# Kernel tuning notes

Measured on AMD Instinct MI355X. Metric: run time of the kernel, lower is better.

The kernel has to match this reference:

```python
import jax, jax.numpy as jnp
import numpy as np

D_EMBED = 1024
N_HEADS = 16
BATCH = 2
SEQ = 2048


def setup_inputs() -> dict:
    key = jax.random.key(0)
    k1, k2, k3 = jax.random.split(key, 3)
    scale = 0.02
    x = jax.random.normal(k1, (BATCH, SEQ, D_EMBED), dtype=jnp.float32)
    w_qkv = jax.random.normal(k2, (D_EMBED, 3 * D_EMBED), dtype=jnp.float32) * scale
    b_qkv = jnp.zeros((3 * D_EMBED,), dtype=jnp.float32)
    w_o = jax.random.normal(k3, (D_EMBED, D_EMBED), dtype=jnp.float32) * scale
    b_o = jnp.zeros((D_EMBED,), dtype=jnp.float32)
    return {"x": x, "w_qkv": w_qkv, "b_qkv": b_qkv, "w_o": w_o, "b_o": b_o}


def reference(x, w_qkv, b_qkv, w_o, b_o):
    bs, sl, ed = x.shape
    nh = N_HEADS
    hd = ed // nh
    # fused QKV projection, split into q, k, v
    qkv = x @ w_qkv + b_qkv                      # [bs, sl, 3*ed]
    q, k, v = jnp.split(qkv, 3, axis=2)
    # [bs, sl, (nh hd)] -> [bs, nh, sl, hd]
    def heads(t):
        return t.reshape(bs, sl, nh, hd).transpose(0, 2, 1, 3)
    q, k, v = heads(q), heads(k), heads(v)
    # scaled dot-product attention with causal mask (full SxS scores, as in the original)
    scores = jnp.einsum('bhqd,bhkd->bhqk', q, k) / jnp.sqrt(jnp.float32(hd))
    causal = jnp.tril(jnp.ones((sl, sl), dtype=bool))
    scores = jnp.where(causal[None, None, :, :], scores, jnp.float32(-jnp.inf))
    attn = jax.nn.softmax(scores, axis=-1)       # dropout p=0 -> identity
    out = jnp.einsum('bhqk,bhkd->bhqd', attn, v) # [bs, nh, sl, hd]
    out = out.transpose(0, 2, 1, 3).reshape(bs, sl, ed)
    return out @ w_o + b_o
```

## Files before the change

kernel.cpp:

```cpp
#include <hip/hip_runtime.h>
#include <hip/hip_bf16.h>

typedef __hip_bfloat16 bf16;
typedef unsigned short u16;
typedef __attribute__((ext_vector_type(8))) short short8;
typedef __attribute__((ext_vector_type(4))) float floatx4;

#define D_EMBED 1024
#define N_HEADS 16
#define HEAD_DIM 64
#define BATCH 2
#define SEQ 2048
#define ROWS (BATCH * SEQ)
#define QKV_COLS (3 * D_EMBED)
#define QSCALE 0.1803368801f

__device__ __forceinline__ void g2l16(const void* g, void* l) {
    __builtin_amdgcn_global_load_lds(
        (const __attribute__((address_space(1))) unsigned int*)g,
        (__attribute__((address_space(3))) unsigned int*)l,
        16, 0, 0);
}

__device__ __forceinline__ u16 f2b_bits(float f) {
    bf16 h = __float2bfloat16(f);
    u16 u;
    __builtin_memcpy(&u, &h, 2);
    return u;
}

__device__ __forceinline__ unsigned pack2(float a, float b) {
    return (unsigned)f2b_bits(a) | ((unsigned)f2b_bits(b) << 16);
}

__device__ __forceinline__ float fexp2(float x) {
#if __has_builtin(__builtin_amdgcn_exp2f)
    return __builtin_amdgcn_exp2f(x);
#else
    return exp2f(x);
#endif
}

__device__ __forceinline__ unsigned permpack(float a, float b) {
#if __has_builtin(__builtin_amdgcn_perm)
    return __builtin_amdgcn_perm(__float_as_uint(b), __float_as_uint(a), 0x07060302u);
#else
    return (__float_as_uint(a) >> 16) | (__float_as_uint(b) & 0xFFFF0000u);
#endif
}

__global__ __launch_bounds__(256)
void prep(const float* __restrict__ x, const float* __restrict__ w_qkv,
          const float* __restrict__ w_o, bf16* __restrict__ xb,
          bf16* __restrict__ wqkvT, bf16* __restrict__ woT)
{
    __shared__ u16 T[64][72];
    const int tid = threadIdx.x;
    const int bid = blockIdx.x;

    if (bid < 4096) {
        const int i = bid * 256 + tid;
        const float4 v = reinterpret_cast<const float4*>(x)[i];
        ushort4 o;
        o.x = f2b_bits(v.x); o.y = f2b_bits(v.y);
        o.z = f2b_bits(v.z); o.w = f2b_bits(v.w);
        reinterpret_cast<ushort4*>(xb)[i] = o;
        return;
    }
    const float* in; u16* out; int R, C, bx, by;
    if (bid < 4864) {
        const int t = bid - 4096;
        in = w_qkv; out = reinterpret_cast<u16*>(wqkvT); R = 1024; C = 3072;
        bx = t % 48; by = t / 48;
    } else {
        const int t = bid - 4864;
        in = w_o; out = reinterpret_cast<u16*>(woT); R = 1024; C = 1024;
        bx = t % 16; by = t / 16;
    }
    const int r0 = by * 64, c0 = bx * 64;
#pragma unroll
    for (int it = 0; it < 4; ++it) {
        const int r = (tid >> 4) + it * 16;
        const int c4 = (tid & 15) * 4;
        const float4 v = *reinterpret_cast<const float4*>(in + (size_t)(r0 + r) * C + c0 + c4);
        T[c4 + 0][r] = f2b_bits(v.x);
        T[c4 + 1][r] = f2b_bits(v.y);
        T[c4 + 2][r] = f2b_bits(v.z);
        T[c4 + 3][r] = f2b_bits(v.w);
    }
    __syncthreads();
#pragma unroll
    for (int it = 0; it < 4; ++it) {
        const int rr = (tid >> 4) + it * 16;
        const int cc4 = (tid & 15) * 4;
        ushort4 o = *reinterpret_cast<const ushort4*>(&T[rr][cc4]);
        *reinterpret_cast<ushort4*>(out + (size_t)(c0 + rr) * R + r0 + cc4) = o;
    }
}

__global__ __launch_bounds__(256)
void gemm_qkv(const bf16* __restrict__ A, const bf16* __restrict__ Bt,
              const float* __restrict__ bias,
              bf16* __restrict__ qb, bf16* __restrict__ kb, bf16* __restrict__ vtb)
{
    __shared__ __align__(16) char smem[16384];
    char* As = smem;
    char* Bs = smem + 8192;

    const int tid = threadIdx.x;
    const int lane = tid & 63, w = tid >> 6;
    const int quad = lane >> 4, l15 = lane & 15;
    const int mw = (w >> 1) * 64, nw = (w & 1) * 64;
    const int blockM = blockIdx.y * 128, blockN = blockIdx.x * 128;

    floatx4 acc[4][4];
#pragma unroll
    for (int i = 0; i < 4; ++i)
#pragma unroll
        for (int j = 0; j < 4; ++j) acc[i][j] = (floatx4){0.f, 0.f, 0.f, 0.f};

    for (int k0 = 0; k0 < 1024; k0 += 32) {
        __syncthreads();
#pragma unroll
        for (int it = 0; it < 2; ++it) {
            const int p = it * 256 + tid;
            const int row = p >> 2, ch = p & 3;
            char* dst = As + (it * 256 + (tid & ~63)) * 16;
            g2l16(A + (size_t)(blockM + row) * 1024 + k0 + ch * 8, dst);
            g2l16(Bt + (size_t)(blockN + row) * 1024 + k0 + ch * 8, dst + 8192);
        }
        __syncthreads();

        short8 af[4], bfr[4];
#pragma unroll
        for (int mi = 0; mi < 4; ++mi)
            af[mi] = *reinterpret_cast<const short8*>(
                As + (mw + mi * 16 + l15) * 64 + quad * 16);
#pragma unroll
        for (int ni = 0; ni < 4; ++ni)
            bfr[ni] = *reinterpret_cast<const short8*>(
                Bs + (nw + ni * 16 + l15) * 64 + quad * 16);
#pragma unroll
        for (int mi = 0; mi < 4; ++mi)
#pragma unroll
            for (int ni = 0; ni < 4; ++ni)
                acc[mi][ni] = __builtin_amdgcn_mfma_f32_16x16x32_bf16(
                    af[mi], bfr[ni], acc[mi][ni], 0, 0, 0);
    }

    __syncthreads();
    u16* W = reinterpret_cast<u16*>(smem + w * 2304);
    const bool isq = (blockN < 1024);
    const bool isv = (blockN >= 2048);

    float bvn[4];
#pragma unroll
    for (int ni = 0; ni < 4; ++ni) bvn[ni] = bias[blockN + nw + ni * 16 + l15];

    if (!isv) {
        bf16* dstbuf = isq ? qb : kb;
        const int coloff = blockN - (isq ? 0 : 1024);
#pragma unroll
        for (int mi = 0; mi < 4; ++mi) {
#pragma unroll
            for (int ni = 0; ni < 4; ++ni) {
#pragma unroll
                for (int r = 0; r < 4; ++r) {
                    float val = acc[mi][ni][r] + bvn[ni];
                    if (isq) val *= QSCALE;
                    W[(quad * 4 + r) * 72 + ni * 16 + l15] = f2b_bits(val);
                }
            }
#pragma unroll
            for (int half = 0; half < 2; ++half) {
                const int idx = half * 64 + lane;
                const int rowL = idx >> 3, ch = idx & 7;
                short8 v = *reinterpret_cast<const short8*>(W + rowL * 72 + ch * 8);
                const int grow = blockM + mw + mi * 16 + rowL;
                const int gcol = coloff + nw + ch * 8;
                *reinterpret_cast<short8*>(
                    reinterpret_cast<u16*>(dstbuf) + (size_t)grow * 1024 + gcol) = v;
            }
        }
    } else {
        const int col0 = blockN - 2048 + nw;
        const int h = col0 >> 6;
        const int bh = (blockM >> 11) * 16 + h;
        const int sb = (blockM & 2047) + mw;
        u16* vdst = reinterpret_cast<u16*>(vtb) + (size_t)bh * 64 * SEQ;
#pragma unroll
        for (int mi = 0; mi < 4; ++mi) {
#pragma unroll
            for (int ni = 0; ni < 4; ++ni) {
#pragma unroll
                for (int r = 0; r < 4; ++r)
                    W[(quad * 4 + r) * 72 + ni * 16 + l15] =
                        f2b_bits(acc[mi][ni][r] + bvn[ni]);
            }
#pragma unroll
            for (int mc = 0; mc < 2; ++mc) {
                u16 tmp[8];
#pragma unroll
                for (int e = 0; e < 8; ++e) tmp[e] = W[(mc * 8 + e) * 72 + lane];
                const int s = sb + mi * 16 + mc * 8;
                *reinterpret_cast<short8*>(vdst + (size_t)lane * SEQ + s) =
                    *reinterpret_cast<const short8*>(tmp);
            }
        }
    }
}

__global__ __launch_bounds__(256)
void gemm_out(const bf16* __restrict__ A, const bf16* __restrict__ Bt,
              const float* __restrict__ bias, float* __restrict__ outf)
{
    __shared__ __align__(16) char smem[12288];
    char* As = smem;
    char* Bs = smem + 8192;

    const int tid = threadIdx.x;
    const int lane = tid & 63, w = tid >> 6;
    const int quad = lane >> 4, l15 = lane & 15;
    const int mw = (w >> 1) * 64, nw = (w & 1) * 32;
    const int blockM = blockIdx.y * 128, blockN = blockIdx.x * 64;

    floatx4 acc[4][2];
#pragma unroll
    for (int i = 0; i < 4; ++i)
#pragma unroll
        for (int j = 0; j < 2; ++j) acc[i][j] = (floatx4){0.f, 0.f, 0.f, 0.f};

    for (int k0 = 0; k0 < 1024; k0 += 32) {
        __syncthreads();
#pragma unroll
        for (int it = 0; it < 2; ++it) {
            const int p = it * 256 + tid;
            const int row = p >> 2, ch = p & 3;
            g2l16(A + (size_t)(blockM + row) * 1024 + k0 + ch * 8,
                  As + (it * 256 + (tid & ~63)) * 16);
        }
        {
            const int row = tid >> 2, ch = tid & 3;
            g2l16(Bt + (size_t)(blockN + row) * 1024 + k0 + ch * 8,
                  Bs + (tid & ~63) * 16);
        }
        __syncthreads();

        short8 af[4], bfr[2];
#pragma unroll
        for (int mi = 0; mi < 4; ++mi)
            af[mi] = *reinterpret_cast<const short8*>(
                As + (mw + mi * 16 + l15) * 64 + quad * 16);
#pragma unroll
        for (int ni = 0; ni < 2; ++ni)
            bfr[ni] = *reinterpret_cast<const short8*>(
                Bs + (nw + ni * 16 + l15) * 64 + quad * 16);
#pragma unroll
        for (int mi = 0; mi < 4; ++mi)
#pragma unroll
            for (int ni = 0; ni < 2; ++ni)
                acc[mi][ni] = __builtin_amdgcn_mfma_f32_16x16x32_bf16(
                    af[mi], bfr[ni], acc[mi][ni], 0, 0, 0);
    }

    float bvn[2];
#pragma unroll
    for (int ni = 0; ni < 2; ++ni) bvn[ni] = bias[blockN + nw + ni * 16 + l15];

#pragma unroll
    for (int mi = 0; mi < 4; ++mi)
#pragma unroll
        for (int r = 0; r < 4; ++r) {
            const int row = blockM + mw + mi * 16 + quad * 4 + r;
#pragma unroll
            for (int ni = 0; ni < 2; ++ni) {
                const int col = blockN + nw + ni * 16 + l15;
                outf[(size_t)row * 1024 + col] = acc[mi][ni][r] + bvn[ni];
            }
        }
}

__global__ __launch_bounds__(256)
void attn_mfma(const bf16* __restrict__ qb, const bf16* __restrict__ kb,
               const bf16* __restrict__ vtb, bf16* __restrict__ ob)
{
    __shared__ __align__(16) char smem[40960];
    char* KV0 = smem;
    char* KV1 = smem + 16384;
    const int tid = threadIdx.x;
    const int lane = tid & 63, w = tid >> 6;
    const int quad = lane >> 4, l15 = lane & 15;
    char* Ps = smem + 32768 + w * 2048;

    const int pi = blockIdx.x;
    const int bh = blockIdx.y;
    const int b = bh >> 4, h = bh & 15;

    const int qtS = pi, qtB = 31 - pi;
    const int q0S = qtS * 64, q0B = qtB * 64;
    const int KT = qtB + 1;
    const int qrowS = q0S + w * 16 + l15;
    const int qrowB = q0B + w * 16 + l15;

    const size_t kvrow = (size_t)b * SEQ;
    const size_t vbase = (size_t)bh * 64 * SEQ;

    const short8 ones = {0x3F80, 0x3F80, 0x3F80, 0x3F80,
                         0x3F80, 0x3F80, 0x3F80, 0x3F80};

    const int row0 = tid >> 3;
    const int lch = (tid & 7) ^ (row0 & 7);
    const int loff0 = (tid & ~63) * 16;
    const int loff1 = loff0 + 4096;
    const bf16* ksrc0 = kb + (kvrow + row0) * D_EMBED + h * 64 + lch * 8;
    const bf16* ksrc1 = ksrc0 + (size_t)32 * D_EMBED;
    const bf16* vsrc0 = vtb + vbase + (size_t)row0 * SEQ + lch * 8;
    const bf16* vsrc1 = vsrc0 + (size_t)32 * SEQ;

    {
        const bf16* qsrcS = qb + (kvrow + q0S + row0) * D_EMBED + h * 64 + lch * 8;
        const bf16* qsrcB = qb + (kvrow + q0B + row0) * D_EMBED + h * 64 + lch * 8;
        g2l16(qsrcS, KV1 + loff0);
        g2l16(qsrcS + (size_t)32 * D_EMBED, KV1 + loff1);
        g2l16(qsrcB, KV1 + 8192 + loff0);
        g2l16(qsrcB + (size_t)32 * D_EMBED, KV1 + 8192 + loff1);
        g2l16(ksrc0, KV0 + loff0);
        g2l16(ksrc1, KV0 + loff1);
        g2l16(vsrc0, KV0 + 8192 + loff0);
        g2l16(vsrc1, KV0 + 8192 + loff1);
    }
    __syncthreads();

    const int qoff = (w * 16 + l15) * 128;
    const int x0 = (quad ^ (l15 & 7)) * 16;
    const int x1 = ((quad + 4) ^ (l15 & 7)) * 16;
    const short8 qS0 = *reinterpret_cast<const short8*>(KV1 + qoff + x0);
    const short8 qS1 = *reinterpret_cast<const short8*>(KV1 + qoff + x1);
    const short8 qB0 = *reinterpret_cast<const short8*>(KV1 + 8192 + qoff + x0);
    const short8 qB1 = *reinterpret_cast<const short8*>(KV1 + 8192 + qoff + x1);
    __syncthreads();

    floatx4 OaccS[4], OaccB[4], LaccS, LaccB;
#pragma unroll
    for (int i = 0; i < 4; ++i) {
        OaccS[i] = (floatx4){0.f, 0.f, 0.f, 0.f};
        OaccB[i] = (floatx4){0.f, 0.f, 0.f, 0.f};
    }
    LaccS = (floatx4){0.f, 0.f, 0.f, 0.f};
    LaccB = (floatx4){0.f, 0.f, 0.f, 0.f};

    auto prefetch = [&](int nkt, char* dst) {
        const size_t ko = (size_t)nkt * 64;
        g2l16(ksrc0 + ko * D_EMBED, dst + loff0);
        g2l16(ksrc1 + ko * D_EMBED, dst + loff1);
        g2l16(vsrc0 + ko, dst + 8192 + loff0);
        g2l16(vsrc1 + ko, dst + 8192 + loff1);
    };

    auto compute = [&](int kt, char* Ks, char* Vs) {
        const int k0 = kt * 64;
        short8 kf[2][4], vf[2][4];
#pragma unroll
        for (int ms = 0; ms < 4; ++ms) {
            const int roff = (ms * 16 + l15) * 128;
            kf[0][ms] = *reinterpret_cast<const short8*>(Ks + roff + x0);
            kf[1][ms] = *reinterpret_cast<const short8*>(Ks + roff + x1);
        }
#pragma unroll
        for (int ks = 0; ks < 2; ++ks)
#pragma unroll
            for (int ds = 0; ds < 4; ++ds)
                vf[ks][ds] = *reinterpret_cast<const short8*>(
                    Vs + (ds * 16 + l15) * 128 + (((quad + ks * 4) ^ (l15 & 7)) * 16));

        {
            floatx4 S[4];
#pragma unroll
            for (int ms = 0; ms < 4; ++ms) {
                floatx4 t = (floatx4){0.f, 0.f, 0.f, 0.f};
                t = __builtin_amdgcn_mfma_f32_16x16x32_bf16(kf[0][ms], qB0, t, 0, 0, 0);
                S[ms] = __builtin_amdgcn_mfma_f32_16x16x32_bf16(kf[1][ms], qB1, t, 0, 0, 0);
            }
            const bool diag = (kt == KT - 1);
#pragma unroll
            for (int ms = 0; ms < 4; ++ms) {
                float p[4];
#pragma unroll
                for (int r = 0; r < 4; ++r) {
                    float s = S[ms][r];
                    if (diag && (k0 + ms * 16 + quad * 4 + r) > qrowB) s = -1e30f;
                    p[r] = fexp2(s);
                }
                const int k = ms * 16 + quad * 4;
                uint2 pw;
                pw.x = permpack(p[0], p[1]);
                pw.y = permpack(p[2], p[3]);
                *reinterpret_cast<uint2*>(Ps + (k >> 3) * 256 + l15 * 16 + (k & 7) * 2) = pw;
            }
#pragma unroll
            for (int ks = 0; ks < 2; ++ks) {
                const short8 pf = *reinterpret_cast<const short8*>(
                    Ps + (ks * 4 + quad) * 256 + l15 * 16);
                LaccB = __builtin_amdgcn_mfma_f32_16x16x32_bf16(ones, pf, LaccB, 0, 0, 0);
#pragma unroll
                for (int ds = 0; ds < 4; ++ds)
                    OaccB[ds] = __builtin_amdgcn_mfma_f32_16x16x32_bf16(
                        vf[ks][ds], pf, OaccB[ds], 0, 0, 0);
            }
        }

        if (kt <= qtS) {
            floatx4 S[4];
#pragma unroll
            for (int ms = 0; ms < 4; ++ms) {
                floatx4 t = (floatx4){0.f, 0.f, 0.f, 0.f};
                t = __builtin_amdgcn_mfma_f32_16x16x32_bf16(kf[0][ms], qS0, t, 0, 0, 0);
                S[ms] = __builtin_amdgcn_mfma_f32_16x16x32_bf16(kf[1][ms], qS1, t, 0, 0, 0);
            }
            const bool diag = (kt == qtS);
#pragma unroll
            for (int ms = 0; ms < 4; ++ms) {
                float p[4];
#pragma unroll
                for (int r = 0; r < 4; ++r) {
                    float s = S[ms][r];
                    if (diag && (k0 + ms * 16 + quad * 4 + r) > qrowS) s = -1e30f;
                    p[r] = fexp2(s);
                }
                const int k = ms * 16 + quad * 4;
                uint2 pw;
                pw.x = permpack(p[0], p[1]);
                pw.y = permpack(p[2], p[3]);
                *reinterpret_cast<uint2*>(Ps + (k >> 3) * 256 + l15 * 16 + (k & 7) * 2) = pw;
            }
#pragma unroll
            for (int ks = 0; ks < 2; ++ks) {
                const short8 pf = *reinterpret_cast<const short8*>(
                    Ps + (ks * 4 + quad) * 256 + l15 * 16);
                LaccS = __builtin_amdgcn_mfma_f32_16x16x32_bf16(ones, pf, LaccS, 0, 0, 0);
#pragma unroll
                for (int ds = 0; ds < 4; ++ds)
                    OaccS[ds] = __builtin_amdgcn_mfma_f32_16x16x32_bf16(
                        vf[ks][ds], pf, OaccS[ds], 0, 0, 0);
            }
        }
    };

#pragma unroll 1
    for (int kt = 0; kt < KT; kt += 2) {
        if (kt + 1 < KT) prefetch(kt + 1, KV1);
        compute(kt, KV0, KV0 + 8192);
        __syncthreads();
        if (kt + 1 >= KT) break;
        if (kt + 2 < KT) prefetch(kt + 2, KV0);
        compute(kt + 1, KV1, KV1 + 8192);
        __syncthreads();
    }

#pragma unroll
    for (int which = 0; which < 2; ++which) {
        const floatx4* Oacc = which ? OaccB : OaccS;
        const float invl = 1.f / (which ? LaccB[0] : LaccS[0]);
        const int q0 = which ? q0B : q0S;
#pragma unroll
        for (int ds = 0; ds < 4; ++ds) {
            const int d = ds * 16 + quad * 4;
            uint2 ow;
            ow.x = pack2(Oacc[ds][0] * invl, Oacc[ds][1] * invl);
            ow.y = pack2(Oacc[ds][2] * invl, Oacc[ds][3] * invl);
            *reinterpret_cast<uint2*>(
                Ps + (d >> 3) * 256 + l15 * 16 + (d & 7) * 2) = ow;
        }
#pragma unroll
        for (int it = 0; it < 2; ++it) {
            const int idx = it * 64 + lane;
            const int ch = idx >> 4, q = idx & 15;
            short8 ov = *reinterpret_cast<const short8*>(Ps + ch * 256 + q * 16);
            *reinterpret_cast<short8*>(
                ob + (kvrow + q0 + w * 16 + q) * D_EMBED + h * 64 + ch * 8) = ov;
        }
    }
}

extern "C" void kernel_launch(void* const* d_in, const int* in_sizes, int n_in,
                              void* d_out, int out_size, void* d_ws, size_t ws_size,
                              hipStream_t stream)
{
    const float* x     = (const float*)d_in[0];
    const float* w_qkv = (const float*)d_in[1];
    const float* b_qkv = (const float*)d_in[2];
    const float* w_o   = (const float*)d_in[3];
    const float* b_o   = (const float*)d_in[4];
    float* out = (float*)d_out;

    bf16* xb     = (bf16*)d_ws;
    bf16* wqkvT  = xb + (size_t)4096 * 1024;
    bf16* woT    = wqkvT + (size_t)3072 * 1024;
    bf16* qbuf   = woT + (size_t)1024 * 1024;
    bf16* kbuf   = qbuf + (size_t)4096 * 1024;
    bf16* vtb    = kbuf + (size_t)4096 * 1024;
    bf16* attnb  = vtb + (size_t)4096 * 1024;

    dim3 blk(256);

    prep<<<dim3(5120), blk, 0, stream>>>(x, w_qkv, w_o, xb, wqkvT, woT);

    gemm_qkv<<<dim3(24, 32), blk, 0, stream>>>(xb, wqkvT, b_qkv, qbuf, kbuf, vtb);

    attn_mfma<<<dim3(16, 32), blk, 0, stream>>>(qbuf, kbuf, vtb, attnb);

    gemm_out<<<dim3(16, 32), blk, 0, stream>>>(attnb, woT, b_o, out);
}
```

Before: 180.7 us.

## Double-buffer LDS tiles in QKV and output projection GEMMs

Both projection GEMMs now use two LDS buffers, so the direct global-to-LDS loads for the next K-slice are issued before the MFMA work on the current slice. This cuts the barriers per K-step from two to one and lets memory latency overlap with compute. It doubles LDS use per block, which may lower occupancy. It also depends on the barrier after each compute to wait for the outstanding async loads before the next buffer is read.

```diff
diff --git a/kernel.cpp b/kernel.cpp
--- a/kernel.cpp
+++ b/kernel.cpp
@@ -103,9 +103,9 @@
               const float* __restrict__ bias,
               bf16* __restrict__ qb, bf16* __restrict__ kb, bf16* __restrict__ vtb)
 {
-    __shared__ __align__(16) char smem[16384];
-    char* As = smem;
-    char* Bs = smem + 8192;
+    __shared__ __align__(16) char smem[32768];
+    char* BUF0 = smem;
+    char* BUF1 = smem + 16384;
 
     const int tid = threadIdx.x;
     const int lane = tid & 63, w = tid >> 6;
@@ -113,42 +113,56 @@
     const int mw = (w >> 1) * 64, nw = (w & 1) * 64;
     const int blockM = blockIdx.y * 128, blockN = blockIdx.x * 128;
 
+    const int row0 = tid >> 2, ch = tid & 3;
+    const int off0 = (tid & ~63) * 16;
+    const bf16* Asrc0 = A + (size_t)(blockM + row0) * 1024 + ch * 8;
+    const bf16* Asrc1 = Asrc0 + (size_t)64 * 1024;
+    const bf16* Bsrc0 = Bt + (size_t)(blockN + row0) * 1024 + ch * 8;
+    const bf16* Bsrc1 = Bsrc0 + (size_t)64 * 1024;
+
+    auto stage = [&](int k0, char* buf) {
+        g2l16(Asrc0 + k0, buf + off0);
+        g2l16(Asrc1 + k0, buf + off0 + 4096);
+        g2l16(Bsrc0 + k0, buf + 8192 + off0);
+        g2l16(Bsrc1 + k0, buf + 8192 + off0 + 4096);
+    };
+
     floatx4 acc[4][4];
 #pragma unroll
     for (int i = 0; i < 4; ++i)
 #pragma unroll
         for (int j = 0; j < 4; ++j) acc[i][j] = (floatx4){0.f, 0.f, 0.f, 0.f};
 
-    for (int k0 = 0; k0 < 1024; k0 += 32) {
-        __syncthreads();
-#pragma unroll
-        for (int it = 0; it < 2; ++it) {
-            const int p = it * 256 + tid;
-            const int row = p >> 2, ch = p & 3;
-            char* dst = As + (it * 256 + (tid & ~63)) * 16;
-            g2l16(A + (size_t)(blockM + row) * 1024 + k0 + ch * 8, dst);
-            g2l16(Bt + (size_t)(blockN + row) * 1024 + k0 + ch * 8, dst + 8192);
-        }
-        __syncthreads();
-
+    auto compute = [&](char* buf) {
         short8 af[4], bfr[4];
 #pragma unroll
         for (int mi = 0; mi < 4; ++mi)
             af[mi] = *reinterpret_cast<const short8*>(
-                As + (mw + mi * 16 + l15) * 64 + quad * 16);
+                buf + (mw + mi * 16 + l15) * 64 + quad * 16);
 #pragma unroll
         for (int ni = 0; ni < 4; ++ni)
             bfr[ni] = *reinterpret_cast<const short8*>(
-                Bs + (nw + ni * 16 + l15) * 64 + quad * 16);
+                buf + 8192 + (nw + ni * 16 + l15) * 64 + quad * 16);
 #pragma unroll
         for (int mi = 0; mi < 4; ++mi)
 #pragma unroll
             for (int ni = 0; ni < 4; ++ni)
                 acc[mi][ni] = __builtin_amdgcn_mfma_f32_16x16x32_bf16(
                     af[mi], bfr[ni], acc[mi][ni], 0, 0, 0);
-    }
-
+    };
+
+    stage(0, BUF0);
     __syncthreads();
+#pragma unroll 1
+    for (int k0 = 0; k0 < 1024; k0 += 64) {
+        if (k0 + 32 < 1024) stage(k0 + 32, BUF1);
+        compute(BUF0);
+        __syncthreads();
+        if (k0 + 64 < 1024) stage(k0 + 64, BUF0);
+        compute(BUF1);
+        __syncthreads();
+    }
+
     u16* W = reinterpret_cast<u16*>(smem + w * 2304);
     const bool isq = (blockN < 1024);
     const bool isv = (blockN >= 2048);
@@ -174,10 +188,10 @@
 #pragma unroll
             for (int half = 0; half < 2; ++half) {
                 const int idx = half * 64 + lane;
-                const int rowL = idx >> 3, ch = idx & 7;
-                short8 v = *reinterpret_cast<const short8*>(W + rowL * 72 + ch * 8);
+                const int rowL = idx >> 3, chh = idx & 7;
+                short8 v = *reinterpret_cast<const short8*>(W + rowL * 72 + chh * 8);
                 const int grow = blockM + mw + mi * 16 + rowL;
-                const int gcol = coloff + nw + ch * 8;
+                const int gcol = coloff + nw + chh * 8;
                 *reinterpret_cast<short8*>(
                     reinterpret_cast<u16*>(dstbuf) + (size_t)grow * 1024 + gcol) = v;
             }
@@ -214,9 +228,9 @@
 void gemm_out(const bf16* __restrict__ A, const bf16* __restrict__ Bt,
               const float* __restrict__ bias, float* __restrict__ outf)
 {
-    __shared__ __align__(16) char smem[12288];
-    char* As = smem;
-    char* Bs = smem + 8192;
+    __shared__ __align__(16) char smem[24576];
+    char* BUF0 = smem;
+    char* BUF1 = smem + 12288;
 
     const int tid = threadIdx.x;
     const int lane = tid & 63, w = tid >> 6;
@@ -224,43 +238,52 @@
     const int mw = (w >> 1) * 64, nw = (w & 1) * 32;
     const int blockM = blockIdx.y * 128, blockN = blockIdx.x * 64;
 
+    const int row0 = tid >> 2, ch = tid & 3;
+    const int off0 = (tid & ~63) * 16;
+    const bf16* Asrc0 = A + (size_t)(blockM + row0) * 1024 + ch * 8;
+    const bf16* Asrc1 = Asrc0 + (size_t)64 * 1024;
+    const bf16* Bsrc0 = Bt + (size_t)(blockN + row0) * 1024 + ch * 8;
+
+    auto stage = [&](int k0, char* buf) {
+        g2l16(Asrc0 + k0, buf + off0);
+        g2l16(Asrc1 + k0, buf + off0 + 4096);
+        g2l16(Bsrc0 + k0, buf + 8192 + off0);
+    };
+
     floatx4 acc[4][2];
 #pragma unroll
     for (int i = 0; i < 4; ++i)
 #pragma unroll
         for (int j = 0; j < 2; ++j) acc[i][j] = (floatx4){0.f, 0.f, 0.f, 0.f};
 
-    for (int k0 = 0; k0 < 1024; k0 += 32) {
-        __syncthreads();
-#pragma unroll
-        for (int it = 0; it < 2; ++it) {
-            const int p = it * 256 + tid;
-            const int row = p >> 2, ch = p & 3;
-            g2l16(A + (size_t)(blockM + row) * 1024 + k0 + ch * 8,
-                  As + (it * 256 + (tid & ~63)) * 16);
-        }
-        {
-            const int row = tid >> 2, ch = tid & 3;
-            g2l16(Bt + (size_t)(blockN + row) * 1024 + k0 + ch * 8,
-                  Bs + (tid & ~63) * 16);
-        }
-        __syncthreads();
-
+    auto compute = [&](char* buf) {
         short8 af[4], bfr[2];
 #pragma unroll
         for (int mi = 0; mi < 4; ++mi)
             af[mi] = *reinterpret_cast<const short8*>(
-                As + (mw + mi * 16 + l15) * 64 + quad * 16);
+                buf + (mw + mi * 16 + l15) * 64 + quad * 16);
 #pragma unroll
         for (int ni = 0; ni < 2; ++ni)
             bfr[ni] = *reinterpret_cast<const short8*>(
-                Bs + (nw + ni * 16 + l15) * 64 + quad * 16);
+                buf + 8192 + (nw + ni * 16 + l15) * 64 + quad * 16);
 #pragma unroll
         for (int mi = 0; mi < 4; ++mi)
 #pragma unroll
             for (int ni = 0; ni < 2; ++ni)
                 acc[mi][ni] = __builtin_amdgcn_mfma_f32_16x16x32_bf16(
                     af[mi], bfr[ni], acc[mi][ni], 0, 0, 0);
+    };
+
+    stage(0, BUF0);
+    __syncthreads();
+#pragma unroll 1
+    for (int k0 = 0; k0 < 1024; k0 += 64) {
+        if (k0 + 32 < 1024) stage(k0 + 32, BUF1);
+        compute(BUF0);
+        __syncthreads();
+        if (k0 + 64 < 1024) stage(k0 + 64, BUF0);
+        compute(BUF1);
+        __syncthreads();
     }
 
     float bvn[2];
```

Measured after the change: 178.9 us. Within noise of the previous version (-1.0%).
